# Optimization experiments

Measured on AMD Instinct MI355X. Metric: run time of the kernel, lower is better.

Reference implementation:

```python
import jax, jax.numpy as jnp
import numpy as np


def setup_inputs() -> dict:
    key = jax.random.key(0)
    ks = jax.random.split(key, 7)
    B, Sq, St, E = 4, 2048, 2048, 512
    s = E ** -0.5
    return {
        "query": jax.random.normal(ks[0], (B, Sq, E), jnp.float32),
        "target": jax.random.normal(ks[1], (B, St, E), jnp.float32),
        "bias": jax.random.normal(ks[2], (1, 1, Sq, St), jnp.float32),
        "Wq": jax.random.normal(ks[3], (E, E), jnp.float32) * s,
        "Wk": jax.random.normal(ks[4], (E, E), jnp.float32) * s,
        "Wv": jax.random.normal(ks[5], (E, E), jnp.float32) * s,
        "Wo": jax.random.normal(ks[6], (E, E), jnp.float32) * s,
    }


def reference(query, target, bias, Wq, Wk, Wv, Wo):
    B, Sq, E = query.shape
    St = target.shape[1]
    H = 8
    hd = E // H  # head_size

    q = query @ Wq   # [B, Sq, E]
    k = target @ Wk  # [B, St, E]
    v = target @ Wv  # [B, St, E]

    # split heads: [B, S, E] -> [B, H, S, hd]
    q = q.reshape(B, Sq, H, hd).transpose(0, 2, 1, 3)
    k = k.reshape(B, St, H, hd).transpose(0, 2, 1, 3)
    v = v.reshape(B, St, H, hd).transpose(0, 2, 1, 3)

    # scores: [B, H, Sq, St]
    weight = jnp.einsum('bhqd,bhtd->bhqt', q, k) / jnp.sqrt(jnp.float32(hd))
    weight = weight + bias
    weight = jax.nn.softmax(weight, axis=-1)
    # dropout: inference mode (training=False) -> identity

    out = jnp.einsum('bhqt,bhtd->bhqd', weight, v)  # [B, H, Sq, hd]
    out = out.transpose(0, 2, 1, 3).reshape(B, Sq, E)  # merge heads
    return out @ Wo
```

## Files before the change

### kernel.cpp

```cpp
#include <hip/hip_runtime.h>
#include <cstdint>

#define B_ 4
#define SQ_ 2048
#define ST_ 2048
#define E_ 512
#define H_ 8
#define HD_ 64
#define LDQ_ 1088
#define QS_ 0.18033688011112043f
#define L2E_ 1.44269504089f
#define BC_ 14.0f

typedef _Float16 f16_t;
typedef _Float16 f16x8 __attribute__((ext_vector_type(8)));
typedef _Float16 f16x4 __attribute__((ext_vector_type(4)));
typedef float f32x4 __attribute__((ext_vector_type(4)));
typedef float f32x16 __attribute__((ext_vector_type(16)));

static __device__ __forceinline__ f16x8 ld8(const f16_t* p) {
  return *reinterpret_cast<const f16x8*>(p);
}

static __device__ __forceinline__ float fast_exp2(float x) {
  float r;
  asm("v_exp_f32 %0, %1" : "=v"(r) : "v"(x));
  return r;
}

static __device__ __forceinline__ unsigned pku(float a, float b) {
  auto h = __builtin_amdgcn_cvt_pkrtz(a, b);
  return __builtin_bit_cast(unsigned, h);
}

static __device__ __forceinline__ void gld16(const f16_t* g, f16_t* l) {
  __builtin_amdgcn_global_load_lds((const __attribute__((address_space(1))) void*)g,
                                   (__attribute__((address_space(3))) void*)l, 16, 0, 0);
}

static __device__ __forceinline__ int swz(int row, int ch) {
  return row * 64 + (((ch ^ (row & 7)) & 7) << 3);
}

__global__ __launch_bounds__(256) void preproc_kernel(const float* __restrict__ query,
                                                      const float* __restrict__ target,
                                                      const float* __restrict__ bias,
                                                      const float* __restrict__ Wq,
                                                      const float* __restrict__ Wk,
                                                      const float* __restrict__ Wv,
                                                      const float* __restrict__ Wo,
                                                      f16_t* __restrict__ qb,
                                                      f16_t* __restrict__ tb,
                                                      f16_t* __restrict__ biasR,
                                                      f16_t* __restrict__ WqkvT,
                                                      f16_t* __restrict__ WoT) {
  __shared__ float smem[64 * 65];
  const int g = blockIdx.x;
  const int tid = threadIdx.x;
  if (g < 8192) {
    const int n4 = (B_ * SQ_ * E_) / 4;
    int i = g * 256 + tid;
    const float* in = query;
    f16_t* out = qb;
    if (i >= n4) { i -= n4; in = target; out = tb; }
    float4 v = reinterpret_cast<const float4*>(in)[i];
    f16x4 o = {(f16_t)v.x, (f16_t)v.y, (f16_t)v.z, (f16_t)v.w};
    reinterpret_cast<f16x4*>(out)[i] = o;
  } else if (g < 9216) {
    const int gb = g - 8192;
    const int t0 = (gb & 31) * 64;
    const int q0 = (gb >> 5) * 64;
    for (int i = tid; i < 64 * 64; i += 256) {
      const int q = i >> 6, t = i & 63;
      smem[q * 65 + t] = bias[(size_t)(q0 + q) * ST_ + t0 + t];
    }
    __syncthreads();
    const int tile_id = tid >> 6;
    const int lane = tid & 63;
    const int qq = tile_id >> 1, tt = tile_id & 1;
    const int q_loc = 32 * qq + (lane & 31);
    const int thl = lane >> 5;
    f16x8 v0, v1;
#pragma unroll
    for (int r = 0; r < 8; ++r) {
      const int t_loc = (r & 3) + 8 * (r >> 2) + 4 * thl + 32 * tt;
      v0[r] = (f16_t)(smem[q_loc * 65 + t_loc] * L2E_ - BC_);
    }
#pragma unroll
    for (int r = 8; r < 16; ++r) {
      const int t_loc = (r & 3) + 8 * (r >> 2) + 4 * thl + 32 * tt;
      v1[r - 8] = (f16_t)(smem[q_loc * 65 + t_loc] * L2E_ - BC_);
    }
    const size_t qb_g = (size_t)(q0 >> 5) + qq, tb_g = (size_t)(t0 >> 5) + tt;
    f16_t* dst = biasR + qb_g * 65536 + tb_g * 1024 + (size_t)lane * 16;
    *reinterpret_cast<f16x8*>(dst) = v0;
    *reinterpret_cast<f16x8*>(dst + 8) = v1;
  } else {
    const int gw = g - 9216;
    const int w = gw >> 8;
    const float* W = (w == 0) ? Wq : (w == 1) ? Wk : (w == 2) ? Wv : Wo;
    f16_t* Wt = (w < 3) ? WqkvT + (size_t)w * E_ * E_ : WoT;
    const float sc = (w == 0) ? QS_ : 1.0f;
    const int bx = (gw & 15) * 32;
    const int by = ((gw >> 4) & 15) * 32;
    const int tx = tid & 31;
    const int ty = tid >> 5;
#pragma unroll
    for (int i = 0; i < 4; ++i)
      smem[(ty + i * 8) * 33 + tx] = W[(size_t)(by + ty + i * 8) * E_ + bx + tx];
    __syncthreads();
#pragma unroll
    for (int i = 0; i < 4; ++i)
      Wt[(size_t)(bx + ty + i * 8) * E_ + by + tx] = (f16_t)(smem[tx * 33 + ty + i * 8] * sc);
  }
}

template <bool OUT_F16, int TN, bool VOUT>
__global__ __launch_bounds__(256) void gemm_bt2_kernel(const f16_t* __restrict__ Aq,
                                                       const f16_t* __restrict__ Akv,
                                                       const f16_t* __restrict__ Bt,
                                                       void* __restrict__ Cv,
                                                       int K, int ldc,
                                                       f16_t* __restrict__ VTout) {
  constexpr int MI = (TN == 128) ? 4 : 2;
  __shared__ f16_t As[2][128 * 32];
  __shared__ f16_t Bs[2][TN * 32];
  const int tid = threadIdx.x;
  const int lane = tid & 63;
  const int wave = tid >> 6;
  const int wm = (TN == 128) ? (wave >> 1) * 64 : wave * 32;
  const int wn = (TN == 128) ? (wave & 1) * 64 : 0;
  const int m0 = blockIdx.y * 128;
  const int n0 = blockIdx.x * TN;
  const int l16 = lane & 15;
  const int quad = lane >> 4;
  const f16_t* A = (n0 < E_) ? Aq : Akv;
  const bool vblk = VOUT && (n0 >= 2 * E_);

  f32x4 acc[MI][4] = {};

  const int r0 = wave * 16 + (lane >> 2);
  const int r1 = (wave + 4) * 16 + (lane >> 2);
  const int c0 = (lane & 3) * 8;
  const f16_t* Ag0 = A + (size_t)(m0 + r0) * K + c0;
  const f16_t* Ag1 = A + (size_t)(m0 + r1) * K + c0;
  const f16_t* Bg0 = Bt + (size_t)(n0 + r0) * K + c0;
  const f16_t* Bg1 = Bt + (size_t)(n0 + r1) * K + c0;
  const int aoff0 = wave * 512 + lane * 8;
  const int aoff1 = (wave + 4) * 512 + lane * 8;

  gld16(Ag0, &As[0][aoff0]);
  gld16(Ag1, &As[0][aoff1]);
  gld16(Bg0, &Bs[0][aoff0]);
  if (TN == 128) gld16(Bg1, &Bs[0][aoff1]);
  int cur = 0;
  __syncthreads();

  for (int k0 = 0; k0 < K; k0 += 32) {
    const int nx = cur ^ 1;
    const int kn = k0 + 32;
    if (kn < K) {
      gld16(Ag0 + kn, &As[nx][aoff0]);
      gld16(Ag1 + kn, &As[nx][aoff1]);
      gld16(Bg0 + kn, &Bs[nx][aoff0]);
      if (TN == 128) gld16(Bg1 + kn, &Bs[nx][aoff1]);
    }
    f16x8 af[MI], bfr[4];
#pragma unroll
    for (int i = 0; i < MI; ++i) af[i] = ld8(&As[cur][(wm + i * 16 + l16) * 32 + quad * 8]);
#pragma unroll
    for (int j = 0; j < 4; ++j) bfr[j] = ld8(&Bs[cur][(wn + j * 16 + l16) * 32 + quad * 8]);
    if (vblk) {
#pragma unroll
      for (int i = 0; i < MI; ++i)
#pragma unroll
        for (int j = 0; j < 4; ++j)
          acc[i][j] = __builtin_amdgcn_mfma_f32_16x16x32_f16(bfr[j], af[i], acc[i][j], 0, 0, 0);
    } else {
#pragma unroll
      for (int i = 0; i < MI; ++i)
#pragma unroll
        for (int j = 0; j < 4; ++j)
          acc[i][j] = __builtin_amdgcn_mfma_f32_16x16x32_f16(af[i], bfr[j], acc[i][j], 0, 0, 0);
    }
    __syncthreads();
    cur = nx;
  }

  if (vblk) {
    const int b = m0 >> 11;
    const int t0g = m0 & 2047;
#pragma unroll
    for (int i = 0; i < MI; ++i)
#pragma unroll
      for (int r = 0; r < 4; ++r) {
#pragma unroll
        for (int j = 0; j < 4; ++j) {
          const int d_g = (n0 - 2 * E_) + wn + j * 16 + quad * 4 + r;
          const size_t t = (size_t)t0g + wm + i * 16 + l16;
          VTout[(size_t)(b * 512 + d_g) * ST_ + t] = (f16_t)acc[i][j][r];
        }
      }
  } else {
#pragma unroll
    for (int i = 0; i < MI; ++i)
#pragma unroll
      for (int r = 0; r < 4; ++r) {
        const size_t row = (size_t)m0 + wm + i * 16 + quad * 4 + r;
#pragma unroll
        for (int j = 0; j < 4; ++j) {
          const size_t col = (size_t)n0 + wn + j * 16 + l16;
          if (OUT_F16)
            reinterpret_cast<f16_t*>(Cv)[row * (size_t)ldc + col] = (f16_t)acc[i][j][r];
          else
            reinterpret_cast<float*>(Cv)[row * (size_t)ldc + col] = acc[i][j][r];
        }
      }
  }
}

__global__ __launch_bounds__(256, 2) void attn_kernel(const f16_t* __restrict__ QKV,
                                                      const f16_t* __restrict__ VT,
                                                      const f16_t* __restrict__ biasR,
                                                      f16_t* __restrict__ O) {
  __shared__ f16_t Ks[2][64 * 64];
  __shared__ f16_t Vs[2][64 * 64];
  const int id = blockIdx.x;
  const int bh = id & 31;
  const int b = bh >> 3, h = bh & 7;
  const int q0 = (id >> 5) * 128;
  const int tid = threadIdx.x;
  const int wave = tid >> 6;
  const int lane = tid & 63;
  const int l32 = lane & 31;
  const int hl = lane >> 5;

  f16x8 bq0, bq1, bq2, bq3;
  {
    const f16_t* qp = QKV + (size_t)(b * SQ_ + q0 + wave * 32 + l32) * LDQ_ + h * HD_ + hl * 8;
    bq0 = ld8(qp);
    bq1 = ld8(qp + 16);
    bq2 = ld8(qp + 32);
    bq3 = ld8(qp + 48);
  }

  const int ch0 = wave * 2, ch1 = ch0 + 1;
  const int rsub = lane >> 3;
  const int csub = (((lane & 7) ^ (lane >> 3)) << 3);
  const f16_t* kg0 = QKV + (size_t)(b * ST_ + ch0 * 8 + rsub) * LDQ_ + E_ + h * HD_ + csub;
  const f16_t* kg1 = QKV + (size_t)(b * ST_ + ch1 * 8 + rsub) * LDQ_ + E_ + h * HD_ + csub;
  const f16_t* vg0 = VT + (size_t)(bh * HD_ + ch0 * 8 + rsub) * ST_ + csub;
  const f16_t* vg1 = VT + (size_t)(bh * HD_ + ch1 * 8 + rsub) * ST_ + csub;
  const int loff0 = ch0 * 512 + lane * 8;
  const int loff1 = ch1 * 512 + lane * 8;

  const f16_t* bb = biasR + (size_t)((q0 >> 5) + wave) * 65536 + (size_t)lane * 16;

  gld16(kg0, &Ks[0][loff0]);
  gld16(kg1, &Ks[0][loff1]);
  gld16(vg0, &Vs[0][loff0]);
  gld16(vg1, &Vs[0][loff1]);
  kg0 += 64 * LDQ_;
  kg1 += 64 * LDQ_;
  vg0 += 64;
  vg1 += 64;
  f16x8 nb00 = ld8(bb), nb01 = ld8(bb + 8);
  f16x8 nb10 = ld8(bb + 1024), nb11 = ld8(bb + 1024 + 8);

  f32x16 facc0 = {}, facc1 = {};
  f32x4 lacc = {};
  int cur = 0;
  __syncthreads();

  auto packA = [&](const f32x16 sv, const int base) -> f16x8 {
    float e[8];
#pragma unroll
    for (int i = 0; i < 8; ++i) {
      e[i] = fast_exp2(sv[base + i]);
      lacc[i & 3] += e[i];
    }
    unsigned u0 = pku(e[0], e[1]);
    unsigned u1 = pku(e[2], e[3]);
    unsigned u2 = pku(e[4], e[5]);
    unsigned u3 = pku(e[6], e[7]);
    asm volatile("v_permlane32_swap_b32 %0, %1" : "+v"(u0), "+v"(u2));
    asm volatile("v_permlane32_swap_b32 %0, %1" : "+v"(u1), "+v"(u3));
    union {
      unsigned u[4];
      f16x8 v;
    } r;
    r.u[0] = u0;
    r.u[1] = u1;
    r.u[2] = u2;
    r.u[3] = u3;
    return r.v;
  };

  for (int t0 = 0; t0 < ST_; t0 += 64) {
    const int nxt = cur ^ 1;
    f16x8 nbn00, nbn01, nbn10, nbn11;
    if (t0 + 64 < ST_) {
      gld16(kg0, &Ks[nxt][loff0]);
      gld16(kg1, &Ks[nxt][loff1]);
      gld16(vg0, &Vs[nxt][loff0]);
      gld16(vg1, &Vs[nxt][loff1]);
      kg0 += 64 * LDQ_;
      kg1 += 64 * LDQ_;
      vg0 += 64;
      vg1 += 64;
      const f16_t* bn = bb + (size_t)((t0 + 64) >> 5) * 1024;
      nbn00 = ld8(bn);
      nbn01 = ld8(bn + 8);
      nbn10 = ld8(bn + 1024);
      nbn11 = ld8(bn + 1024 + 8);
    }

    f32x16 s0, s1;
    __builtin_amdgcn_s_setprio(1);
    {
      f32x16 c;
#pragma unroll
      for (int i = 0; i < 8; ++i) {
        c[i] = (float)nb00[i];
        c[i + 8] = (float)nb01[i];
      }
      c = __builtin_amdgcn_mfma_f32_32x32x16_f16(ld8(&Ks[cur][swz(l32, 0 + hl)]), bq0, c, 0, 0, 0);
      c = __builtin_amdgcn_mfma_f32_32x32x16_f16(ld8(&Ks[cur][swz(l32, 2 + hl)]), bq1, c, 0, 0, 0);
      c = __builtin_amdgcn_mfma_f32_32x32x16_f16(ld8(&Ks[cur][swz(l32, 4 + hl)]), bq2, c, 0, 0, 0);
      c = __builtin_amdgcn_mfma_f32_32x32x16_f16(ld8(&Ks[cur][swz(l32, 6 + hl)]), bq3, c, 0, 0, 0);
      s0 = c;
    }
    {
      f32x16 c;
#pragma unroll
      for (int i = 0; i < 8; ++i) {
        c[i] = (float)nb10[i];
        c[i + 8] = (float)nb11[i];
      }
      const int rw = 32 + l32;
      c = __builtin_amdgcn_mfma_f32_32x32x16_f16(ld8(&Ks[cur][swz(rw, 0 + hl)]), bq0, c, 0, 0, 0);
      c = __builtin_amdgcn_mfma_f32_32x32x16_f16(ld8(&Ks[cur][swz(rw, 2 + hl)]), bq1, c, 0, 0, 0);
      c = __builtin_amdgcn_mfma_f32_32x32x16_f16(ld8(&Ks[cur][swz(rw, 4 + hl)]), bq2, c, 0, 0, 0);
      c = __builtin_amdgcn_mfma_f32_32x32x16_f16(ld8(&Ks[cur][swz(rw, 6 + hl)]), bq3, c, 0, 0, 0);
      s1 = c;
    }
    __builtin_amdgcn_s_setprio(0);

    const f16x8 A0 = packA(s0, 0);
    const f16x8 A1 = packA(s0, 8);
    const f16x8 A2 = packA(s1, 0);
    const f16x8 A3 = packA(s1, 8);

    __builtin_amdgcn_s_setprio(1);
#define PVSTEP(Af, ks)                                                                            \
  facc0 = __builtin_amdgcn_mfma_f32_32x32x16_f16((Af), ld8(&Vs[cur][swz(l32, (ks)*2 + hl)]),      \
                                                 facc0, 0, 0, 0);                                 \
  facc1 = __builtin_amdgcn_mfma_f32_32x32x16_f16((Af), ld8(&Vs[cur][swz(32 + l32, (ks)*2 + hl)]), \
                                                 facc1, 0, 0, 0);
    PVSTEP(A0, 0)
    PVSTEP(A1, 1)
    PVSTEP(A2, 2)
    PVSTEP(A3, 3)
#undef PVSTEP
    __builtin_amdgcn_s_setprio(0);

    __syncthreads();

    if (t0 + 64 < ST_) {
      nb00 = nbn00;
      nb01 = nbn01;
      nb10 = nbn10;
      nb11 = nbn11;
    }
    cur = nxt;
  }

  float l_i = lacc[0] + lacc[1] + lacc[2] + lacc[3];
  l_i += __shfl_xor(l_i, 32);
  const float inv = 1.0f / l_i;
#pragma unroll
  for (int r = 0; r < 16; ++r) {
    const int qr = (r & 3) + 8 * (r >> 2) + 4 * hl;
    const float ir = __shfl(inv, qr);
    f16_t* op = O + (size_t)(b * SQ_ + q0 + wave * 32 + qr) * E_ + h * HD_ + l32;
    op[0] = (f16_t)(facc0[r] * ir);
    op[32] = (f16_t)(facc1[r] * ir);
  }
}

extern "C" void kernel_launch(void* const* d_in, const int* in_sizes, int n_in,
                              void* d_out, int out_size, void* d_ws, size_t ws_size,
                              hipStream_t stream) {
  (void)in_sizes; (void)n_in; (void)out_size; (void)ws_size;
  const float* query = (const float*)d_in[0];
  const float* target = (const float*)d_in[1];
  const float* bias = (const float*)d_in[2];
  const float* Wq = (const float*)d_in[3];
  const float* Wk = (const float*)d_in[4];
  const float* Wv = (const float*)d_in[5];
  const float* Wo = (const float*)d_in[6];

  char* ws = (char*)d_ws;
  const size_t ACT = (size_t)B_ * SQ_ * E_;
  const size_t ACT_B = ACT * sizeof(f16_t);
  const size_t BIAS_B = (size_t)SQ_ * ST_ * sizeof(f16_t);
  const size_t W_B = (size_t)E_ * E_ * sizeof(f16_t);

  f16_t* qb = (f16_t*)(ws);
  f16_t* tb = (f16_t*)(ws + ACT_B);
  f16_t* biasR = (f16_t*)(ws + 2 * ACT_B);
  f16_t* WqkvT = (f16_t*)(ws + 2 * ACT_B + BIAS_B);
  f16_t* WoT = WqkvT + 3 * (size_t)E_ * E_;
  f16_t* QKV = (f16_t*)(ws + 2 * ACT_B + BIAS_B + 4 * W_B);
  f16_t* VT = QKV + (size_t)B_ * SQ_ * LDQ_;
  f16_t* attn = tb;

  dim3 blk(256);
  preproc_kernel<<<dim3(10240), blk, 0, stream>>>(query, target, bias, Wq, Wk, Wv, Wo, qb, tb,
                                                  biasR, WqkvT, WoT);

  gemm_bt2_kernel<true, 128, true><<<dim3(3 * E_ / 128, B_ * SQ_ / 128), blk, 0, stream>>>(
      qb, tb, WqkvT, QKV, E_, LDQ_, VT);

  attn_kernel<<<dim3(SQ_ / 128 * B_ * H_), blk, 0, stream>>>(QKV, VT, biasR, attn);

  gemm_bt2_kernel<false, 64, false><<<dim3(E_ / 64, B_ * SQ_ / 128), blk, 0, stream>>>(
      attn, attn, WoT, (void*)d_out, E_, E_, nullptr);
}
```

Baseline: 202.5 us.

## Rework projection GEMM with 64-wide K tiles, XOR-swizzled LDS and 128x64 blocks

Replaces the projection GEMM with a version that stages 64-deep K slices in shared memory and stores them with an XOR swizzle, which is meant to avoid LDS bank conflicts and halve the number of barriers per K. The QKV projection now uses 128x64 output tiles instead of 128x128, doubling its grid size for better CU occupancy at the cost of less reuse of A per block. Shared memory per block grows, which may reduce how many blocks fit on a CU.

```diff
diff --git a/kernel.cpp b/kernel.cpp
--- a/kernel.cpp
+++ b/kernel.cpp
@@ -115,73 +115,77 @@
   }
 }
 
-template <bool OUT_F16, int TN, bool VOUT>
-__global__ __launch_bounds__(256) void gemm_bt2_kernel(const f16_t* __restrict__ Aq,
+template <bool OUT_F16, bool VOUT>
+__global__ __launch_bounds__(256) void gemm_bt3_kernel(const f16_t* __restrict__ Aq,
                                                        const f16_t* __restrict__ Akv,
                                                        const f16_t* __restrict__ Bt,
                                                        void* __restrict__ Cv,
                                                        int K, int ldc,
                                                        f16_t* __restrict__ VTout) {
-  constexpr int MI = (TN == 128) ? 4 : 2;
-  __shared__ f16_t As[2][128 * 32];
-  __shared__ f16_t Bs[2][TN * 32];
+  __shared__ f16_t As[2][128 * 64];
+  __shared__ f16_t Bs[2][64 * 64];
   const int tid = threadIdx.x;
   const int lane = tid & 63;
   const int wave = tid >> 6;
-  const int wm = (TN == 128) ? (wave >> 1) * 64 : wave * 32;
-  const int wn = (TN == 128) ? (wave & 1) * 64 : 0;
+  const int wm = wave * 32;
   const int m0 = blockIdx.y * 128;
-  const int n0 = blockIdx.x * TN;
+  const int n0 = blockIdx.x * 64;
   const int l16 = lane & 15;
   const int quad = lane >> 4;
   const f16_t* A = (n0 < E_) ? Aq : Akv;
   const bool vblk = VOUT && (n0 >= 2 * E_);
 
-  f32x4 acc[MI][4] = {};
-
-  const int r0 = wave * 16 + (lane >> 2);
-  const int r1 = (wave + 4) * 16 + (lane >> 2);
-  const int c0 = (lane & 3) * 8;
-  const f16_t* Ag0 = A + (size_t)(m0 + r0) * K + c0;
-  const f16_t* Ag1 = A + (size_t)(m0 + r1) * K + c0;
-  const f16_t* Bg0 = Bt + (size_t)(n0 + r0) * K + c0;
-  const f16_t* Bg1 = Bt + (size_t)(n0 + r1) * K + c0;
-  const int aoff0 = wave * 512 + lane * 8;
-  const int aoff1 = (wave + 4) * 512 + lane * 8;
-
-  gld16(Ag0, &As[0][aoff0]);
-  gld16(Ag1, &As[0][aoff1]);
-  gld16(Bg0, &Bs[0][aoff0]);
-  if (TN == 128) gld16(Bg1, &Bs[0][aoff1]);
+  f32x4 acc[2][4] = {};
+
+  const int rsub = lane >> 3;
+  const int csub = (((lane & 7) ^ (lane >> 3)) << 3);
+  const f16_t* Ag[4];
+#pragma unroll
+  for (int i = 0; i < 4; ++i)
+    Ag[i] = A + (size_t)(m0 + wave * 32 + i * 8 + rsub) * K + csub;
+  const f16_t* Bg[2];
+#pragma unroll
+  for (int i = 0; i < 2; ++i)
+    Bg[i] = Bt + (size_t)(n0 + wave * 16 + i * 8 + rsub) * K + csub;
+  const int adst = wave * 32 * 64 + lane * 8;
+  const int bdst = wave * 16 * 64 + lane * 8;
+
+#pragma unroll
+  for (int i = 0; i < 4; ++i) gld16(Ag[i], &As[0][adst + i * 512]);
+#pragma unroll
+  for (int i = 0; i < 2; ++i) gld16(Bg[i], &Bs[0][bdst + i * 512]);
   int cur = 0;
   __syncthreads();
 
-  for (int k0 = 0; k0 < K; k0 += 32) {
+  for (int k0 = 0; k0 < K; k0 += 64) {
     const int nx = cur ^ 1;
-    const int kn = k0 + 32;
+    const int kn = k0 + 64;
     if (kn < K) {
-      gld16(Ag0 + kn, &As[nx][aoff0]);
-      gld16(Ag1 + kn, &As[nx][aoff1]);
-      gld16(Bg0 + kn, &Bs[nx][aoff0]);
-      if (TN == 128) gld16(Bg1 + kn, &Bs[nx][aoff1]);
-    }
-    f16x8 af[MI], bfr[4];
-#pragma unroll
-    for (int i = 0; i < MI; ++i) af[i] = ld8(&As[cur][(wm + i * 16 + l16) * 32 + quad * 8]);
-#pragma unroll
-    for (int j = 0; j < 4; ++j) bfr[j] = ld8(&Bs[cur][(wn + j * 16 + l16) * 32 + quad * 8]);
-    if (vblk) {
-#pragma unroll
-      for (int i = 0; i < MI; ++i)
-#pragma unroll
-        for (int j = 0; j < 4; ++j)
-          acc[i][j] = __builtin_amdgcn_mfma_f32_16x16x32_f16(bfr[j], af[i], acc[i][j], 0, 0, 0);
-    } else {
-#pragma unroll
-      for (int i = 0; i < MI; ++i)
-#pragma unroll
-        for (int j = 0; j < 4; ++j)
-          acc[i][j] = __builtin_amdgcn_mfma_f32_16x16x32_f16(af[i], bfr[j], acc[i][j], 0, 0, 0);
+#pragma unroll
+      for (int i = 0; i < 4; ++i) gld16(Ag[i] + kn, &As[nx][adst + i * 512]);
+#pragma unroll
+      for (int i = 0; i < 2; ++i) gld16(Bg[i] + kn, &Bs[nx][bdst + i * 512]);
+    }
+#pragma unroll
+    for (int s = 0; s < 2; ++s) {
+      f16x8 af[2], bfr[4];
+#pragma unroll
+      for (int i = 0; i < 2; ++i) af[i] = ld8(&As[cur][swz(wm + i * 16 + l16, s * 4 + quad)]);
+#pragma unroll
+      for (int j = 0; j < 4; ++j) bfr[j] = ld8(&Bs[cur][swz(j * 16 + l16, s * 4 + quad)]);
+      if (vblk) {
+#pragma unroll
+        for (int i = 0; i < 2; ++i)
+#pragma unroll
+          for (int j = 0; j < 4; ++j)
+            acc[i][j] = __builtin_amdgcn_mfma_f32_16x16x32_f16(bfr[j], af[i], acc[i][j], 0, 0, 0);
+      } else {
+#pragma unroll
+        for (int i = 0; i < 2; ++i)
+#pragma unroll
+          for (int j = 0; j < 4; ++j)
+            acc[i][j] = __builtin_amdgcn_mfma_f32_16x16x32_f16(af[i], bfr[j], acc[i][j], 0, 0, 0);
+      }
     }
     __syncthreads();
     cur = nx;
@@ -191,25 +195,24 @@
     const int b = m0 >> 11;
     const int t0g = m0 & 2047;
 #pragma unroll
-    for (int i = 0; i < MI; ++i)
-#pragma unroll
-      for (int r = 0; r < 4; ++r) {
+    for (int i = 0; i < 2; ++i)
+#pragma unroll
+      for (int r = 0; r < 4; ++r)
 #pragma unroll
         for (int j = 0; j < 4; ++j) {
-          const int d_g = (n0 - 2 * E_) + wn + j * 16 + quad * 4 + r;
+          const int d_g = (n0 - 2 * E_) + j * 16 + quad * 4 + r;
           const size_t t = (size_t)t0g + wm + i * 16 + l16;
           VTout[(size_t)(b * 512 + d_g) * ST_ + t] = (f16_t)acc[i][j][r];
         }
-      }
   } else {
 #pragma unroll
-    for (int i = 0; i < MI; ++i)
+    for (int i = 0; i < 2; ++i)
 #pragma unroll
       for (int r = 0; r < 4; ++r) {
         const size_t row = (size_t)m0 + wm + i * 16 + quad * 4 + r;
 #pragma unroll
         for (int j = 0; j < 4; ++j) {
-          const size_t col = (size_t)n0 + wn + j * 16 + l16;
+          const size_t col = (size_t)n0 + j * 16 + l16;
           if (OUT_F16)
             reinterpret_cast<f16_t*>(Cv)[row * (size_t)ldc + col] = (f16_t)acc[i][j][r];
           else
@@ -419,11 +422,11 @@
   preproc_kernel<<<dim3(10240), blk, 0, stream>>>(query, target, bias, Wq, Wk, Wv, Wo, qb, tb,
                                                   biasR, WqkvT, WoT);
 
-  gemm_bt2_kernel<true, 128, true><<<dim3(3 * E_ / 128, B_ * SQ_ / 128), blk, 0, stream>>>(
+  gemm_bt3_kernel<true, true><<<dim3(3 * E_ / 64, B_ * SQ_ / 128), blk, 0, stream>>>(
       qb, tb, WqkvT, QKV, E_, LDQ_, VT);
 
   attn_kernel<<<dim3(SQ_ / 128 * B_ * H_), blk, 0, stream>>>(QKV, VT, biasR, attn);
 
-  gemm_bt2_kernel<false, 64, false><<<dim3(E_ / 64, B_ * SQ_ / 128), blk, 0, stream>>>(
+  gemm_bt3_kernel<false, false><<<dim3(E_ / 64, B_ * SQ_ / 128), blk, 0, stream>>>(
       attn, attn, WoT, (void*)d_out, E_, E_, nullptr);
 }
```

Result: faster. 193.2 us (-4.6%).
